# Optimization experiments

Measured on AMD Instinct MI355X. Metric: run time of the kernel, lower is better.

## Reference

```python
import jax, jax.numpy as jnp
import numpy as np

EMBED = 1024
HEADS = 16
HEAD_DIM = EMBED // HEADS


def setup_inputs() -> dict:
    key = jax.random.key(0)
    ks = jax.random.split(key, 8)
    N, S = 4, 2048
    values = jax.random.normal(ks[0], (N, S, EMBED), dtype=jnp.float32)
    queries = jax.random.normal(ks[1], (N, S, EMBED), dtype=jnp.float32)
    keys = jax.random.normal(ks[2], (N, S, EMBED), dtype=jnp.float32)
    mask = jax.random.randint(ks[3], (N, 1, S, S), 0, 2, dtype=jnp.int32)
    sc = 1.0 / np.sqrt(HEAD_DIM)
    Wv = jax.random.normal(ks[4], (HEAD_DIM, HEAD_DIM), dtype=jnp.float32) * sc
    Wk = jax.random.normal(ks[5], (HEAD_DIM, HEAD_DIM), dtype=jnp.float32) * sc
    Wq = jax.random.normal(ks[6], (HEAD_DIM, HEAD_DIM), dtype=jnp.float32) * sc
    Wo = jax.random.normal(ks[7], (EMBED, EMBED), dtype=jnp.float32) * (1.0 / np.sqrt(EMBED))
    bo = jnp.zeros((EMBED,), dtype=jnp.float32)
    return {"values": values, "queries": queries, "keys": keys, "mask": mask,
            "Wv": Wv, "Wk": Wk, "Wq": Wq, "Wo": Wo, "bo": bo}


def reference(values, queries, keys, mask, Wv, Wk, Wq, Wo, bo):
    N, S, _ = queries.shape
    # split heads: (N, len, H, D)
    v = values.reshape(N, -1, HEADS, HEAD_DIM)
    k = keys.reshape(N, -1, HEADS, HEAD_DIM)
    q = queries.reshape(N, -1, HEADS, HEAD_DIM)
    # per-head linear projections (nn.Linear: y = x @ W.T, no bias)
    v = jnp.einsum('nlhd,ed->nlhe', v, Wv)
    k = jnp.einsum('nlhd,ed->nlhe', k, Wk)
    q = jnp.einsum('nlhd,ed->nlhe', q, Wq)
    # energy: (N, H, q_len, k_len)
    energy = jnp.einsum('nqhd,nkhd->nhqk', q, k)
    energy = jnp.where(mask == 0, jnp.float32(-1e20), energy)
    # non-standard scale: sqrt(embed_size), applied after masking
    attn = jax.nn.softmax(energy / jnp.sqrt(jnp.float32(EMBED)), axis=3)
    out = jnp.einsum('nhql,nlhd->nqhd', attn, v).reshape(N, S, EMBED)
    return out @ Wo.T + bo
```

## Files before the change

kernel.cpp:

```cpp
#include <hip/hip_runtime.h>
#include <hip/hip_bf16.h>

#define NBATCH 4
#define SEQ    2048
#define EMBED  1024
#define HEADS  16
#define HD     64

typedef __attribute__((ext_vector_type(8))) short bf16x8;
typedef __attribute__((ext_vector_type(4))) float f32x4;

__device__ __forceinline__ short f2bf(float f) {
  union { float f; unsigned u; } v; v.f = f;
  unsigned r = v.u + 0x7fffu + ((v.u >> 16) & 1u);
  return (short)(r >> 16);
}

__device__ __forceinline__ unsigned pkbf(float a, float b) {
#if __has_builtin(__builtin_amdgcn_cvt_pk_bf16_f32)
  typedef __attribute__((ext_vector_type(2))) __bf16 bf16x2_t;
  bf16x2_t r = __builtin_amdgcn_cvt_pk_bf16_f32(a, b);
  union { bf16x2_t v; unsigned u; } cv; cv.v = r; return cv.u;
#else
  return (unsigned)(unsigned short)f2bf(a) | ((unsigned)(unsigned short)f2bf(b) << 16);
#endif
}

typedef __attribute__((address_space(1))) const void gas_void;
typedef __attribute__((address_space(3))) void las_void;
__device__ __forceinline__ void glds16(const void* g, void* l) {
  __builtin_amdgcn_global_load_lds((gas_void*)g, (las_void*)l, 16, 0, 0);
}

__global__ __launch_bounds__(256) void cvt_all(
    const float* __restrict__ Wo, const float* __restrict__ Wq,
    const float* __restrict__ Wk, const float* __restrict__ Wv,
    short* __restrict__ dWo, short* __restrict__ dWq,
    short* __restrict__ dWk, short* __restrict__ dWv)
{
  int e = (blockIdx.x * 256 + threadIdx.x) * 4;
  const float* src; short* dst; int off;
  if (e < EMBED * EMBED) { src = Wo; dst = dWo; off = e; }
  else {
    int j = e - EMBED * EMBED;
    if      (j < 4096)  { src = Wq; dst = dWq; off = j; }
    else if (j < 8192)  { src = Wk; dst = dWk; off = j - 4096; }
    else if (j < 12288) { src = Wv; dst = dWv; off = j - 8192; }
    else return;
  }
  float4 v = *(const float4*)(src + off);
  ushort4 p;
  p.x = (unsigned short)f2bf(v.x);
  p.y = (unsigned short)f2bf(v.y);
  p.z = (unsigned short)f2bf(v.z);
  p.w = (unsigned short)f2bf(v.w);
  *(ushort4*)(dst + off) = p;
}

__global__ __launch_bounds__(256) void mask_pack(const int* __restrict__ mask,
                                                 unsigned long long* __restrict__ bits) {
  long long t = (long long)blockIdx.x * 256 + threadIdx.x;
  int lane = threadIdx.x & 63;
  int m = mask[t];
  unsigned long long b = __ballot(m != 0);
  if (lane == 0) bits[t >> 6] = b;
}

__global__ __launch_bounds__(256) void proj_kernel(
    const float* __restrict__ srcQ, const float* __restrict__ srcK, const float* __restrict__ srcV,
    const short* __restrict__ WbQ, const short* __restrict__ WbK, const short* __restrict__ WbV,
    short* __restrict__ Qp, short* __restrict__ Kp, short* __restrict__ Vt)
{
  int rt = blockIdx.x;
  int h  = blockIdx.y;
  int mz = blockIdx.z;
  const float* src = (mz == 0) ? srcQ : ((mz == 1) ? srcK : srcV);
  const short* Wb  = (mz == 0) ? WbQ : ((mz == 1) ? WbK : WbV);

  __shared__ __align__(16) short At[64][72];

  int tid = threadIdx.x;
  int r0 = rt * 64;
  for (int idx = tid; idx < 64 * 16; idx += 256) {
    int row = idx >> 4;
    int c4  = idx & 15;
    const float4* p = (const float4*)(src + (long long)(r0 + row) * EMBED + h * HD + c4 * 4);
    float4 v = *p;
    At[row][c4 * 4 + 0] = f2bf(v.x);
    At[row][c4 * 4 + 1] = f2bf(v.y);
    At[row][c4 * 4 + 2] = f2bf(v.z);
    At[row][c4 * 4 + 3] = f2bf(v.w);
  }
  __syncthreads();

  int lane = tid & 63, w = tid >> 6, quad = lane >> 4, l15 = lane & 15;

  bf16x8 af0 = *(const bf16x8*)&At[w * 16 + l15][quad * 8];
  bf16x8 af1 = *(const bf16x8*)&At[w * 16 + l15][32 + quad * 8];

  f32x4 acc[4];
  for (int cg = 0; cg < 4; cg++) {
    acc[cg] = (f32x4){0.f, 0.f, 0.f, 0.f};
    bf16x8 b0 = *(const bf16x8*)(Wb + (cg * 16 + l15) * 64 + quad * 8);
    bf16x8 b1 = *(const bf16x8*)(Wb + (cg * 16 + l15) * 64 + 32 + quad * 8);
    acc[cg] = __builtin_amdgcn_mfma_f32_16x16x32_bf16(af0, b0, acc[cg], 0, 0, 0);
    acc[cg] = __builtin_amdgcn_mfma_f32_16x16x32_bf16(af1, b1, acc[cg], 0, 0, 0);
  }

  int rloc = w * 16 + quad * 4;
  if (mz < 2) {
    short* dst = (mz == 0) ? Qp : Kp;
    for (int cg = 0; cg < 4; cg++) {
      for (int reg = 0; reg < 4; reg++) {
        int r = r0 + rloc + reg;
        int n = r >> 11, s = r & 2047;
        dst[((long long)(n * HEADS + h) * SEQ + s) * HD + cg * 16 + l15] = f2bf(acc[cg][reg]);
      }
    }
  } else {
    int r = r0 + rloc;
    int n = r >> 11, s = r & 2047;
    for (int cg = 0; cg < 4; cg++) {
      int d = cg * 16 + l15;
      ushort4 pk;
      pk.x = (unsigned short)f2bf(acc[cg][0]);
      pk.y = (unsigned short)f2bf(acc[cg][1]);
      pk.z = (unsigned short)f2bf(acc[cg][2]);
      pk.w = (unsigned short)f2bf(acc[cg][3]);
      *(ushort4*)(Vt + ((long long)(n * HEADS + h) * HD + d) * SEQ + s) = pk;
    }
  }
}

__global__ __launch_bounds__(256) void attn_kernel(
    const short* __restrict__ Qp, const short* __restrict__ Kp, const short* __restrict__ Vt,
    const unsigned long long* __restrict__ mbits, short* __restrict__ AO)
{
  int qt = blockIdx.x, h = blockIdx.y, nb = blockIdx.z;
  int q0 = qt * 64;

  __shared__ __align__(16) short KtL[64 * 64];
  __shared__ __align__(16) short VsL[64 * 64];
  __shared__ __align__(16) short Pls[4][16][72];

  int tid = threadIdx.x, lane = tid & 63, w = tid >> 6, quad = lane >> 4, l15 = lane & 15;
  int g8 = lane & 7, r8 = lane >> 3;
  int swz = g8 ^ r8;
  int s3 = l15 & 7;
  int o0 = (quad ^ s3) * 16;
  int o1 = ((quad + 4) ^ s3) * 16;

  long long nh = (long long)(nb * HEADS + h);
  const char* Kb = (const char*)(Kp + nh * SEQ * HD);
  const char* Vb = (const char*)(Vt + nh * HD * SEQ);
  const short* Qbase = Qp + (nh * SEQ + q0) * HD;

  int qrow = q0 + w * 16 + l15;

  int kgo = (w * 16 + r8) * 128 + swz * 16;
  int vgo = (w * 16 + r8) * 4096 + swz * 16;
  unsigned klo = (unsigned)(w * 16) * 128;

  const unsigned long long* mptr = mbits + ((long long)nb * SEQ + qrow) * 32;

  bf16x8 qf0 = *(const bf16x8*)(Qbase + (w * 16 + l15) * HD + quad * 8);
  bf16x8 qf1 = *(const bf16x8*)(Qbase + (w * 16 + l15) * HD + 32 + quad * 8);

  f32x4 O[4];
#pragma unroll
  for (int i = 0; i < 4; i++) O[i] = (f32x4){0.f, 0.f, 0.f, 0.f};
  float lsum = 0.f;

  const float C2 = 0.04508422f;

  for (int kt = 0; kt < 32; kt++) {
    int k0 = kt * 64;
    __syncthreads();
    {
      const char* kg = Kb + k0 * 128 + kgo;
      const char* vg = Vb + k0 * 2 + vgo;
      glds16(kg,         (char*)KtL + klo);
      glds16(kg + 1024,  (char*)KtL + klo + 1024);
      glds16(vg,         (char*)VsL + klo);
      glds16(vg + 32768, (char*)VsL + klo + 1024);
    }
    unsigned long long mrow = mptr[kt];
    __syncthreads();

    const char* KB = (const char*)KtL;
    f32x4 sA[4];
#pragma unroll
    for (int cg = 0; cg < 4; cg++) {
      bf16x8 kf0 = *(const bf16x8*)(KB + (cg * 16 + l15) * 128 + o0);
      bf16x8 kf1 = *(const bf16x8*)(KB + (cg * 16 + l15) * 128 + o1);
      f32x4 a = (f32x4){0.f, 0.f, 0.f, 0.f};
      a = __builtin_amdgcn_mfma_f32_16x16x32_bf16(kf0, qf0, a, 0, 0, 0);
      a = __builtin_amdgcn_mfma_f32_16x16x32_bf16(kf1, qf1, a, 0, 0, 0);
      sA[cg] = a;
    }

    unsigned mlo = (unsigned)mrow, mhi = (unsigned)(mrow >> 32);
    unsigned sh = (unsigned)(quad * 4);
    unsigned nibs[4];
    nibs[0] = (mlo >> sh) & 0xFu;
    nibs[1] = (mlo >> (sh + 16)) & 0xFu;
    nibs[2] = (mhi >> sh) & 0xFu;
    nibs[3] = (mhi >> (sh + 16)) & 0xFu;

    float ssum = 0.f;
#pragma unroll
    for (int cg = 0; cg < 4; cg++) {
#pragma unroll
      for (int r = 0; r < 4; r++) {
        float p = __builtin_amdgcn_exp2f(sA[cg][r] * C2);
        p = (nibs[cg] & (1u << r)) ? p : 0.f;
        sA[cg][r] = p;
        ssum += p;
      }
    }
    lsum += ssum;

#pragma unroll
    for (int cg = 0; cg < 4; cg++) {
      uint2 pk;
      pk.x = pkbf(sA[cg][0], sA[cg][1]);
      pk.y = pkbf(sA[cg][2], sA[cg][3]);
      *(uint2*)&Pls[w][l15][cg * 16 + quad * 4] = pk;
    }

    bf16x8 pa0 = *(const bf16x8*)&Pls[w][l15][quad * 8];
    bf16x8 pa1 = *(const bf16x8*)&Pls[w][l15][32 + quad * 8];

    const char* VB = (const char*)VsL;
#pragma unroll
    for (int cg = 0; cg < 4; cg++) {
      bf16x8 vf0 = *(const bf16x8*)(VB + (cg * 16 + l15) * 128 + o0);
      bf16x8 vf1 = *(const bf16x8*)(VB + (cg * 16 + l15) * 128 + o1);
      O[cg] = __builtin_amdgcn_mfma_f32_16x16x32_bf16(vf0, pa0, O[cg], 0, 0, 0);
      O[cg] = __builtin_amdgcn_mfma_f32_16x16x32_bf16(vf1, pa1, O[cg], 0, 0, 0);
    }
  }

  lsum += __shfl_xor(lsum, 16);
  lsum += __shfl_xor(lsum, 32);
  float inv = 1.f / lsum;
  short* aoRow = AO + ((long long)nb * SEQ + qrow) * EMBED + h * HD;
#pragma unroll
  for (int cg = 0; cg < 4; cg++) {
    uint2 pk;
    pk.x = pkbf(O[cg][0] * inv, O[cg][1] * inv);
    pk.y = pkbf(O[cg][2] * inv, O[cg][3] * inv);
    *(uint2*)(aoRow + cg * 16 + quad * 4) = pk;
  }
}

__global__ __launch_bounds__(256) void outproj_kernel(
    const short* __restrict__ AO, const short* __restrict__ Wob,
    const float* __restrict__ bo, float* __restrict__ out)
{
  int rt = blockIdx.x, ct = blockIdx.y;
  __shared__ __align__(16) short AtL[64 * 64];
  __shared__ __align__(16) short BtL[64 * 64];
  int tid = threadIdx.x, lane = tid & 63, w = tid >> 6, quad = lane >> 4, l15 = lane & 15;
  int g8 = lane & 7, r8 = lane >> 3;
  int swz = g8 ^ r8;
  int s3 = l15 & 7;
  int o0 = (quad ^ s3) * 16;
  int o1 = ((quad + 4) ^ s3) * 16;
  int r0 = rt * 64, c0 = ct * 64;

  const char* Abase = (const char*)AO  + ((long long)(r0 + w * 16 + r8) * EMBED) * 2 + swz * 16;
  const char* Bbase = (const char*)Wob + ((long long)(c0 + w * 16 + r8) * EMBED) * 2 + swz * 16;
  unsigned lbo = (unsigned)(w * 16) * 128;

  f32x4 acc[4];
  for (int i = 0; i < 4; i++) acc[i] = (f32x4){0.f, 0.f, 0.f, 0.f};

  for (int kc = 0; kc < 16; kc++) {
    __syncthreads();
    {
      const char* ag = Abase + kc * 128;
      const char* bg = Bbase + kc * 128;
      glds16(ag,                 (char*)AtL + lbo);
      glds16(ag + 8 * EMBED * 2, (char*)AtL + lbo + 1024);
      glds16(bg,                 (char*)BtL + lbo);
      glds16(bg + 8 * EMBED * 2, (char*)BtL + lbo + 1024);
    }
    __syncthreads();

    const char* AB = (const char*)AtL;
    const char* BB = (const char*)BtL;
    bf16x8 a0 = *(const bf16x8*)(AB + (w * 16 + l15) * 128 + o0);
    bf16x8 a1 = *(const bf16x8*)(AB + (w * 16 + l15) * 128 + o1);
#pragma unroll
    for (int cg = 0; cg < 4; cg++) {
      bf16x8 b0 = *(const bf16x8*)(BB + (cg * 16 + l15) * 128 + o0);
      bf16x8 b1 = *(const bf16x8*)(BB + (cg * 16 + l15) * 128 + o1);
      acc[cg] = __builtin_amdgcn_mfma_f32_16x16x32_bf16(a0, b0, acc[cg], 0, 0, 0);
      acc[cg] = __builtin_amdgcn_mfma_f32_16x16x32_bf16(a1, b1, acc[cg], 0, 0, 0);
    }
  }

  for (int cg = 0; cg < 4; cg++) {
    float b = bo[c0 + cg * 16 + l15];
    for (int reg = 0; reg < 4; reg++) {
      int r = r0 + w * 16 + quad * 4 + reg;
      out[(long long)r * EMBED + c0 + cg * 16 + l15] = acc[cg][reg] + b;
    }
  }
}

extern "C" void kernel_launch(void* const* d_in, const int* in_sizes, int n_in,
                              void* d_out, int out_size, void* d_ws, size_t ws_size,
                              hipStream_t stream) {
  const float* values  = (const float*)d_in[0];
  const float* queries = (const float*)d_in[1];
  const float* keys    = (const float*)d_in[2];
  const int*   mask    = (const int*)d_in[3];
  const float* Wv = (const float*)d_in[4];
  const float* Wk = (const float*)d_in[5];
  const float* Wq = (const float*)d_in[6];
  const float* Wo = (const float*)d_in[7];
  const float* bo = (const float*)d_in[8];
  float* out = (float*)d_out;

  char* ws = (char*)d_ws;
  size_t off = 0;
  const size_t PROJ_BYTES = (size_t)NBATCH * HEADS * SEQ * HD * 2;
  short* Qp = (short*)(ws + off); off += PROJ_BYTES;
  short* Kp = (short*)(ws + off); off += PROJ_BYTES;
  short* Vt = (short*)(ws + off); off += PROJ_BYTES;
  short* AO = (short*)(ws + off); off += PROJ_BYTES;
  unsigned long long* mbits = (unsigned long long*)(ws + off);
  off += (size_t)NBATCH * SEQ * (SEQ / 64) * 8;
  short* Wob = (short*)(ws + off); off += (size_t)EMBED * EMBED * 2;
  short* WbQ = (short*)(ws + off); off += HD * HD * 2;
  short* WbK = (short*)(ws + off); off += HD * HD * 2;
  short* WbV = (short*)(ws + off); off += HD * HD * 2;

  cvt_all<<<dim3((EMBED * EMBED + 3 * HD * HD) / 4 / 256), dim3(256), 0, stream>>>(
      Wo, Wq, Wk, Wv, Wob, WbQ, WbK, WbV);

  mask_pack<<<dim3((NBATCH * SEQ * SEQ) / 256), dim3(256), 0, stream>>>(mask, mbits);

  proj_kernel<<<dim3((NBATCH * SEQ) / 64, HEADS, 3), dim3(256), 0, stream>>>(
      queries, keys, values, WbQ, WbK, WbV, Qp, Kp, Vt);

  attn_kernel<<<dim3(SEQ / 64, HEADS, NBATCH), dim3(256), 0, stream>>>(Qp, Kp, Vt, mbits, AO);

  outproj_kernel<<<dim3((NBATCH * SEQ) / 64, EMBED / 64), dim3(256), 0, stream>>>(AO, Wob, bo, out);
}
```

Baseline: 387.1 us.

## Fold softmax scale into Wq, enlarge attention and out-proj tiles

Pre-multiplies Wq by the log2e/sqrt(E) constant during weight conversion so the attention inner loop can drop a multiply before exp2. Attention blocks now cover 128 queries with 512 threads, so each K/V tile load is shared by twice as many queries. The output projection moves to 128x128 tiles with a 4x4 MFMA register block per wave to raise operand reuse. Projection stores use packed bf16 conversion. Larger tiles raise register and LDS pressure and reduce the block count, which may lower occupancy.

```diff
diff --git a/kernel.cpp b/kernel.cpp
--- a/kernel.cpp
+++ b/kernel.cpp
@@ -32,6 +32,8 @@
   __builtin_amdgcn_global_load_lds((gas_void*)g, (las_void*)l, 16, 0, 0);
 }
 
+#define C2 0.04508422f
+
 __global__ __launch_bounds__(256) void cvt_all(
     const float* __restrict__ Wo, const float* __restrict__ Wq,
     const float* __restrict__ Wk, const float* __restrict__ Wv,
@@ -39,21 +41,21 @@
     short* __restrict__ dWk, short* __restrict__ dWv)
 {
   int e = (blockIdx.x * 256 + threadIdx.x) * 4;
-  const float* src; short* dst; int off;
+  const float* src; short* dst; int off; float sc = 1.0f;
   if (e < EMBED * EMBED) { src = Wo; dst = dWo; off = e; }
   else {
     int j = e - EMBED * EMBED;
-    if      (j < 4096)  { src = Wq; dst = dWq; off = j; }
+    if      (j < 4096)  { src = Wq; dst = dWq; off = j; sc = C2; }
     else if (j < 8192)  { src = Wk; dst = dWk; off = j - 4096; }
     else if (j < 12288) { src = Wv; dst = dWv; off = j - 8192; }
     else return;
   }
   float4 v = *(const float4*)(src + off);
   ushort4 p;
-  p.x = (unsigned short)f2bf(v.x);
-  p.y = (unsigned short)f2bf(v.y);
-  p.z = (unsigned short)f2bf(v.z);
-  p.w = (unsigned short)f2bf(v.w);
+  p.x = (unsigned short)f2bf(v.x * sc);
+  p.y = (unsigned short)f2bf(v.y * sc);
+  p.z = (unsigned short)f2bf(v.z * sc);
+  p.w = (unsigned short)f2bf(v.w * sc);
   *(ushort4*)(dst + off) = p;
 }
 
@@ -84,12 +86,11 @@
   for (int idx = tid; idx < 64 * 16; idx += 256) {
     int row = idx >> 4;
     int c4  = idx & 15;
-    const float4* p = (const float4*)(src + (long long)(r0 + row) * EMBED + h * HD + c4 * 4);
-    float4 v = *p;
-    At[row][c4 * 4 + 0] = f2bf(v.x);
-    At[row][c4 * 4 + 1] = f2bf(v.y);
-    At[row][c4 * 4 + 2] = f2bf(v.z);
-    At[row][c4 * 4 + 3] = f2bf(v.w);
+    float4 v = *(const float4*)(src + (long long)(r0 + row) * EMBED + h * HD + c4 * 4);
+    uint2 pk2;
+    pk2.x = pkbf(v.x, v.y);
+    pk2.y = pkbf(v.z, v.w);
+    *(uint2*)&At[row][c4 * 4] = pk2;
   }
   __syncthreads();
 
@@ -122,26 +123,24 @@
     int n = r >> 11, s = r & 2047;
     for (int cg = 0; cg < 4; cg++) {
       int d = cg * 16 + l15;
-      ushort4 pk;
-      pk.x = (unsigned short)f2bf(acc[cg][0]);
-      pk.y = (unsigned short)f2bf(acc[cg][1]);
-      pk.z = (unsigned short)f2bf(acc[cg][2]);
-      pk.w = (unsigned short)f2bf(acc[cg][3]);
-      *(ushort4*)(Vt + ((long long)(n * HEADS + h) * HD + d) * SEQ + s) = pk;
-    }
-  }
-}
-
-__global__ __launch_bounds__(256) void attn_kernel(
+      uint2 pk2;
+      pk2.x = pkbf(acc[cg][0], acc[cg][1]);
+      pk2.y = pkbf(acc[cg][2], acc[cg][3]);
+      *(uint2*)(Vt + ((long long)(n * HEADS + h) * HD + d) * SEQ + s) = pk2;
+    }
+  }
+}
+
+__global__ __launch_bounds__(512) void attn_kernel(
     const short* __restrict__ Qp, const short* __restrict__ Kp, const short* __restrict__ Vt,
     const unsigned long long* __restrict__ mbits, short* __restrict__ AO)
 {
   int qt = blockIdx.x, h = blockIdx.y, nb = blockIdx.z;
-  int q0 = qt * 64;
+  int q0 = qt * 128;
 
   __shared__ __align__(16) short KtL[64 * 64];
   __shared__ __align__(16) short VsL[64 * 64];
-  __shared__ __align__(16) short Pls[4][16][72];
+  __shared__ __align__(16) short Pls[8][16][72];
 
   int tid = threadIdx.x, lane = tid & 63, w = tid >> 6, quad = lane >> 4, l15 = lane & 15;
   int g8 = lane & 7, r8 = lane >> 3;
@@ -157,9 +156,9 @@
 
   int qrow = q0 + w * 16 + l15;
 
-  int kgo = (w * 16 + r8) * 128 + swz * 16;
-  int vgo = (w * 16 + r8) * 4096 + swz * 16;
-  unsigned klo = (unsigned)(w * 16) * 128;
+  int kgo = (w * 8 + r8) * 128 + swz * 16;
+  int vgo = (w * 8 + r8) * 4096 + swz * 16;
+  unsigned klo = (unsigned)(w * 8) * 128;
 
   const unsigned long long* mptr = mbits + ((long long)nb * SEQ + qrow) * 32;
 
@@ -170,20 +169,12 @@
 #pragma unroll
   for (int i = 0; i < 4; i++) O[i] = (f32x4){0.f, 0.f, 0.f, 0.f};
   float lsum = 0.f;
-
-  const float C2 = 0.04508422f;
 
   for (int kt = 0; kt < 32; kt++) {
     int k0 = kt * 64;
     __syncthreads();
-    {
-      const char* kg = Kb + k0 * 128 + kgo;
-      const char* vg = Vb + k0 * 2 + vgo;
-      glds16(kg,         (char*)KtL + klo);
-      glds16(kg + 1024,  (char*)KtL + klo + 1024);
-      glds16(vg,         (char*)VsL + klo);
-      glds16(vg + 32768, (char*)VsL + klo + 1024);
-    }
+    glds16(Kb + k0 * 128 + kgo, (char*)KtL + klo);
+    glds16(Vb + k0 * 2   + vgo, (char*)VsL + klo);
     unsigned long long mrow = mptr[kt];
     __syncthreads();
 
@@ -212,7 +203,7 @@
     for (int cg = 0; cg < 4; cg++) {
 #pragma unroll
       for (int r = 0; r < 4; r++) {
-        float p = __builtin_amdgcn_exp2f(sA[cg][r] * C2);
+        float p = __builtin_amdgcn_exp2f(sA[cg][r]);
         p = (nibs[cg] & (1u << r)) ? p : 0.f;
         sA[cg][r] = p;
         ssum += p;
@@ -259,54 +250,72 @@
     const float* __restrict__ bo, float* __restrict__ out)
 {
   int rt = blockIdx.x, ct = blockIdx.y;
-  __shared__ __align__(16) short AtL[64 * 64];
-  __shared__ __align__(16) short BtL[64 * 64];
+  __shared__ __align__(16) short AtL[128 * 64];
+  __shared__ __align__(16) short BtL[128 * 64];
+
   int tid = threadIdx.x, lane = tid & 63, w = tid >> 6, quad = lane >> 4, l15 = lane & 15;
   int g8 = lane & 7, r8 = lane >> 3;
   int swz = g8 ^ r8;
   int s3 = l15 & 7;
   int o0 = (quad ^ s3) * 16;
   int o1 = ((quad + 4) ^ s3) * 16;
-  int r0 = rt * 64, c0 = ct * 64;
-
-  const char* Abase = (const char*)AO  + ((long long)(r0 + w * 16 + r8) * EMBED) * 2 + swz * 16;
-  const char* Bbase = (const char*)Wob + ((long long)(c0 + w * 16 + r8) * EMBED) * 2 + swz * 16;
-  unsigned lbo = (unsigned)(w * 16) * 128;
-
-  f32x4 acc[4];
-  for (int i = 0; i < 4; i++) acc[i] = (f32x4){0.f, 0.f, 0.f, 0.f};
+
+  int r0 = rt * 128, c0 = ct * 128;
+  int wr = (w >> 1) * 64, wc = (w & 1) * 64;
+
+  const char* Abase = (const char*)AO  + (long long)(r0 + w * 8 + r8) * 2048 + swz * 16;
+  const char* Bbase = (const char*)Wob + (long long)(c0 + w * 8 + r8) * 2048 + swz * 16;
+  unsigned lbase = (unsigned)(w * 8) * 128;
+
+  f32x4 acc[4][4];
+#pragma unroll
+  for (int mi = 0; mi < 4; mi++)
+#pragma unroll
+    for (int ni = 0; ni < 4; ni++) acc[mi][ni] = (f32x4){0.f, 0.f, 0.f, 0.f};
 
   for (int kc = 0; kc < 16; kc++) {
     __syncthreads();
-    {
-      const char* ag = Abase + kc * 128;
-      const char* bg = Bbase + kc * 128;
-      glds16(ag,                 (char*)AtL + lbo);
-      glds16(ag + 8 * EMBED * 2, (char*)AtL + lbo + 1024);
-      glds16(bg,                 (char*)BtL + lbo);
-      glds16(bg + 8 * EMBED * 2, (char*)BtL + lbo + 1024);
+#pragma unroll
+    for (int i = 0; i < 4; i++) {
+      glds16(Abase + (long long)i * 32 * 2048 + kc * 128, (char*)AtL + lbase + i * 32 * 128);
+      glds16(Bbase + (long long)i * 32 * 2048 + kc * 128, (char*)BtL + lbase + i * 32 * 128);
     }
     __syncthreads();
 
     const char* AB = (const char*)AtL;
     const char* BB = (const char*)BtL;
-    bf16x8 a0 = *(const bf16x8*)(AB + (w * 16 + l15) * 128 + o0);
-    bf16x8 a1 = *(const bf16x8*)(AB + (w * 16 + l15) * 128 + o1);
-#pragma unroll
-    for (int cg = 0; cg < 4; cg++) {
-      bf16x8 b0 = *(const bf16x8*)(BB + (cg * 16 + l15) * 128 + o0);
-      bf16x8 b1 = *(const bf16x8*)(BB + (cg * 16 + l15) * 128 + o1);
-      acc[cg] = __builtin_amdgcn_mfma_f32_16x16x32_bf16(a0, b0, acc[cg], 0, 0, 0);
-      acc[cg] = __builtin_amdgcn_mfma_f32_16x16x32_bf16(a1, b1, acc[cg], 0, 0, 0);
-    }
-  }
-
-  for (int cg = 0; cg < 4; cg++) {
-    float b = bo[c0 + cg * 16 + l15];
-    for (int reg = 0; reg < 4; reg++) {
-      int r = r0 + w * 16 + quad * 4 + reg;
-      out[(long long)r * EMBED + c0 + cg * 16 + l15] = acc[cg][reg] + b;
-    }
+    bf16x8 af[4][2], bf[4][2];
+#pragma unroll
+    for (int mi = 0; mi < 4; mi++) {
+      int r = wr + mi * 16 + l15;
+      af[mi][0] = *(const bf16x8*)(AB + r * 128 + o0);
+      af[mi][1] = *(const bf16x8*)(AB + r * 128 + o1);
+    }
+#pragma unroll
+    for (int ni = 0; ni < 4; ni++) {
+      int r = wc + ni * 16 + l15;
+      bf[ni][0] = *(const bf16x8*)(BB + r * 128 + o0);
+      bf[ni][1] = *(const bf16x8*)(BB + r * 128 + o1);
+    }
+#pragma unroll
+    for (int mi = 0; mi < 4; mi++)
+#pragma unroll
+      for (int ni = 0; ni < 4; ni++) {
+        acc[mi][ni] = __builtin_amdgcn_mfma_f32_16x16x32_bf16(af[mi][0], bf[ni][0], acc[mi][ni], 0, 0, 0);
+        acc[mi][ni] = __builtin_amdgcn_mfma_f32_16x16x32_bf16(af[mi][1], bf[ni][1], acc[mi][ni], 0, 0, 0);
+      }
+  }
+
+#pragma unroll
+  for (int ni = 0; ni < 4; ni++) {
+    float b = bo[c0 + wc + ni * 16 + l15];
+#pragma unroll
+    for (int mi = 0; mi < 4; mi++)
+#pragma unroll
+      for (int reg = 0; reg < 4; reg++) {
+        int r = r0 + wr + mi * 16 + quad * 4 + reg;
+        out[(long long)r * EMBED + c0 + wc + ni * 16 + l15] = acc[mi][ni][reg] + b;
+      }
   }
 }
 
@@ -346,7 +355,7 @@
   proj_kernel<<<dim3((NBATCH * SEQ) / 64, HEADS, 3), dim3(256), 0, stream>>>(
       queries, keys, values, WbQ, WbK, WbV, Qp, Kp, Vt);
 
-  attn_kernel<<<dim3(SEQ / 64, HEADS, NBATCH), dim3(256), 0, stream>>>(Qp, Kp, Vt, mbits, AO);
-
-  outproj_kernel<<<dim3((NBATCH * SEQ) / 64, EMBED / 64), dim3(256), 0, stream>>>(AO, Wob, bo, out);
-}
+  attn_kernel<<<dim3(SEQ / 128, HEADS, NBATCH), dim3(512), 0, stream>>>(Qp, Kp, Vt, mbits, AO);
+
+  outproj_kernel<<<dim3((NBATCH * SEQ) / 128, EMBED / 128), dim3(256), 0, stream>>>(AO, Wob, bo, out);
+}
```

Result: faster. 378.3 us (-2.3%).
